# Performance work log

Hardware: AMD Instinct MI355X
Metric: run time of the kernel (lower is better)

Reference implementation:

```python
import jax, jax.numpy as jnp
import numpy as np

NUM_HEADS = 4
NUM_GROUPS = 32
EPS = 1e-5


def setup_inputs() -> dict:
    key = jax.random.key(0)
    ks = jax.random.split(key, 4)
    ch = 256
    x = jax.random.normal(ks[0], (16, ch, 32, 32), dtype=jnp.float32)
    gn_w = jnp.ones((ch,), jnp.float32)
    gn_b = jnp.zeros((ch,), jnp.float32)
    # conv1x1 weights, kaiming-ish scale
    qkv_w = jax.random.normal(ks[1], (3 * ch, ch), dtype=jnp.float32) / np.sqrt(ch)
    qkv_b = jnp.zeros((3 * ch,), jnp.float32)
    proj_w = jax.random.normal(ks[2], (ch, ch), dtype=jnp.float32) / np.sqrt(ch)
    proj_b = jnp.zeros((ch,), jnp.float32)
    return {"x": x, "gn_w": gn_w, "gn_b": gn_b, "qkv_w": qkv_w,
            "qkv_b": qkv_b, "proj_w": proj_w, "proj_b": proj_b}


def _group_norm(x, w, b):
    bsz, c, h, wd = x.shape
    g = NUM_GROUPS
    xg = x.reshape(bsz, g, c // g, h, wd)
    mean = xg.mean(axis=(2, 3, 4), keepdims=True)
    var = xg.var(axis=(2, 3, 4), keepdims=True)
    xg = (xg - mean) * jax.lax.rsqrt(var + EPS)
    return xg.reshape(bsz, c, h, wd) * w[None, :, None, None] + b[None, :, None, None]


def reference(x, gn_w, gn_b, qkv_w, qkv_b, proj_w, proj_b):
    b, c, h, w = x.shape
    hd = c // NUM_HEADS
    scale = hd ** (-0.5)
    y = _group_norm(x, gn_w, gn_b)
    # 1x1 conv == channel matmul
    qkv = jnp.einsum('oc,bchw->bohw', qkv_w, y) + qkv_b[None, :, None, None]
    q, k, v = jnp.split(qkv, 3, axis=1)
    q = q.reshape(b, NUM_HEADS, hd, h * w)
    k = k.reshape(b, NUM_HEADS, hd, h * w)
    v = v.reshape(b, NUM_HEADS, hd, h * w)
    attn = jnp.einsum('bhdi,bhdj->bhij', q * scale, k)
    attn = jax.nn.softmax(attn, axis=-1)
    out = jnp.einsum('bhij,bhdj->bhdi', attn, v)
    out = out.reshape(b, c, h, w)
    out = jnp.einsum('oc,bchw->bohw', proj_w, out) + proj_b[None, :, None, None]
    return x + out
```

## Files before the change

kernel.cpp:

```cpp
#include <hip/hip_runtime.h>
#include <cstddef>

#define B_   16
#define C_   256
#define HW_  1024
#define NH_  4
#define NG_  32
#define CPG_ 8
#define CS_  0.18033688f

typedef __attribute__((ext_vector_type(8))) short bf16x8;
typedef __attribute__((ext_vector_type(4))) short s16x4;
typedef __attribute__((ext_vector_type(8))) _Float16 f16x8;
typedef __attribute__((ext_vector_type(4))) float f32x4;

#define MFMA16B(a, b, c) __builtin_amdgcn_mfma_f32_16x16x32_bf16(a, b, c, 0, 0, 0)
#define MFMA16H(a, b, c) __builtin_amdgcn_mfma_f32_16x16x32_f16(a, b, c, 0, 0, 0)

#if __has_builtin(__builtin_amdgcn_mfma_f32_16x16x16bf16_1k)
#define HAVE_MFMA16K16 1
#define MFMA16B4(a, b, c) __builtin_amdgcn_mfma_f32_16x16x16bf16_1k(a, b, c, 0, 0, 0)
#else
#define HAVE_MFMA16K16 0
#endif

__device__ __forceinline__ float bf2f(unsigned short h) {
    unsigned int u = ((unsigned int)h) << 16;
    return __builtin_bit_cast(float, u);
}
__device__ __forceinline__ unsigned short f2bf(float f) {
    unsigned int u = __builtin_bit_cast(unsigned int, f);
    u += 0x7FFFu + ((u >> 16) & 1u);
    return (unsigned short)(u >> 16);
}
#if __has_builtin(__builtin_amdgcn_cvt_pk_bf16_f32)
__device__ __forceinline__ unsigned packbf(float a, float b) {
    auto v = __builtin_amdgcn_cvt_pk_bf16_f32(a, b);
    return __builtin_bit_cast(unsigned, v);
}
#else
__device__ __forceinline__ unsigned packbf(float a, float b) {
    unsigned ua = __builtin_bit_cast(unsigned, a) + 0x8000u;
    unsigned ub = __builtin_bit_cast(unsigned, b) + 0x8000u;
    return __builtin_amdgcn_perm(ub, ua, 0x07060302u);
}
#endif
__device__ __forceinline__ unsigned pkh(float a, float b) {
    auto h2 = __builtin_amdgcn_cvt_pkrtz(a, b);
    return __builtin_bit_cast(unsigned, h2);
}

__global__ __launch_bounds__(256) void gn_wcvt_kernel(
    const float* __restrict__ x,
    const float* __restrict__ gw,
    const float* __restrict__ gb,
    float2* __restrict__ scsh,
    const float* __restrict__ qw, const float* __restrict__ pw,
    unsigned short* __restrict__ oq, unsigned short* __restrict__ op)
{
    if (blockIdx.x >= 512) {
        int i = (blockIdx.x - 512) * 256 + threadIdx.x;
        const float* s; unsigned short* d; int j;
        if (i < 49152) { s = qw; d = oq; j = i; }
        else           { s = pw; d = op; j = i - 49152; }
        float4 f = ((const float4*)s)[j];
        uint2 u = {pkh(f.x, f.y), pkh(f.z, f.w)};
        *(uint2*)&d[(size_t)j * 4] = u;
        return;
    }
    int blk = blockIdx.x;
    const float* xg = x + (size_t)blk * CPG_ * HW_;
    const int N = CPG_ * HW_;

    float s = 0.f, ss = 0.f;
    for (int e = threadIdx.x * 4; e < N; e += 1024) {
        float4 v4 = *(const float4*)&xg[e];
        s  += v4.x + v4.y + v4.z + v4.w;
        ss += v4.x * v4.x + v4.y * v4.y + v4.z * v4.z + v4.w * v4.w;
    }
    #pragma unroll
    for (int off = 32; off > 0; off >>= 1) {
        s  += __shfl_down(s, off, 64);
        ss += __shfl_down(ss, off, 64);
    }
    __shared__ float red[8];
    __shared__ float2 stf;
    int lane = threadIdx.x & 63, wv = threadIdx.x >> 6;
    if (lane == 0) { red[wv] = s; red[4 + wv] = ss; }
    __syncthreads();
    if (threadIdx.x == 0) {
        float S  = red[0] + red[1] + red[2] + red[3];
        float SS = red[4] + red[5] + red[6] + red[7];
        float mean = S / (float)N;
        float var  = SS / (float)N - mean * mean;
        stf = make_float2(mean, rsqrtf(var + 1e-5f));
    }
    __syncthreads();
    if (threadIdx.x < 8) {
        int ch = (blk & 31) * CPG_ + threadIdx.x;
        float sc = stf.y * gw[ch];
        float sh = gb[ch] - stf.x * sc;
        scsh[blk * 8 + threadIdx.x] = make_float2(sc, sh);
    }
}

__global__ __launch_bounds__(256) void qkv_mfma_kernel(
    const unsigned short* __restrict__ W16,
    const float* __restrict__ Xf,
    const float* __restrict__ bias,
    const float2* __restrict__ scsh,
    unsigned short* __restrict__ qT,
    unsigned short* __restrict__ kT,
    unsigned short* __restrict__ vN)
{
    const int M = 768, K = 256, N = 1024;
    __shared__ union {
        struct { unsigned short A[2][128][40]; unsigned short Bt[2][64][40]; } st;
        unsigned short nd[2][64][72];
        unsigned short mn[128][72];
    } L;

    const int b  = blockIdx.z;
    const int m0 = blockIdx.y * 128, n0 = blockIdx.x * 64;
    const int t  = threadIdx.x;
    const int l15 = t & 15, quad = (t >> 4) & 3;
    const int wave = t >> 6, wm = wave >> 1, wn = wave & 1;

    union HF { uint4 q; f16x8 v; };

    f32x4 acc[4][2];
    #pragma unroll
    for (int mt = 0; mt < 4; ++mt)
        #pragma unroll
        for (int nt = 0; nt < 2; ++nt)
            acc[mt][nt] = (f32x4){0.f, 0.f, 0.f, 0.f};

    const int ar = t >> 1, akh = (t & 1) * 16;
    const int bn = t & 63, bkb = t >> 6;

    uint4 pa0, pa1;
    float pv[8];
    float2 ss[8];

    auto PREF = [&](int k0) {
        const unsigned short* wp = &W16[(size_t)(m0 + ar) * K + k0 + akh];
        pa0 = *(const uint4*)wp;
        pa1 = *(const uint4*)(wp + 8);
        int ch = k0 + bkb * 8;
        const float* xp = &Xf[((size_t)b * K + ch) * N + n0 + bn];
        #pragma unroll
        for (int j = 0; j < 8; ++j) pv[j] = xp[(size_t)j * N];
        const float4* sp = (const float4*)&scsh[b * C_ + ch];
        #pragma unroll
        for (int q2 = 0; q2 < 4; ++q2) ((float4*)ss)[q2] = sp[q2];
    };

    PREF(0);
    #pragma unroll 1
    for (int it = 0; it < 8; ++it) {
        const int bsel = it & 1;
        *(uint4*)&L.st.A[bsel][ar][akh]     = pa0;
        *(uint4*)&L.st.A[bsel][ar][akh + 8] = pa1;
        {
            float v[8];
            #pragma unroll
            for (int j = 0; j < 8; ++j) v[j] = pv[j] * ss[j].x + ss[j].y;
            uint4 bw = {pkh(v[0], v[1]), pkh(v[2], v[3]), pkh(v[4], v[5]), pkh(v[6], v[7])};
            *(uint4*)&L.st.Bt[bsel][bn][bkb * 8] = bw;
        }
        __syncthreads();
        if (it + 1 < 8) PREF((it + 1) * 32);
        HF af[4], bfv[2];
        #pragma unroll
        for (int mt = 0; mt < 4; ++mt)
            af[mt].q = *(const uint4*)&L.st.A[bsel][wm * 64 + mt * 16 + l15][quad * 8];
        #pragma unroll
        for (int nt = 0; nt < 2; ++nt)
            bfv[nt].q = *(const uint4*)&L.st.Bt[bsel][wn * 32 + nt * 16 + l15][quad * 8];
        #pragma unroll
        for (int mt = 0; mt < 4; ++mt)
            #pragma unroll
            for (int nt = 0; nt < 2; ++nt)
                acc[mt][nt] = MFMA16H(af[mt].v, bfv[nt].v, acc[mt][nt]);
    }
    __syncthreads();

    if (m0 < 512) {
        const float qsc = (m0 < 256) ? CS_ : 1.f;
        #pragma unroll
        for (int mt = 0; mt < 4; ++mt)
            #pragma unroll
            for (int rr = 0; rr < 4; ++rr) {
                int dl = mt * 16 + quad * 4 + rr;
                float bv = bias[m0 + wm * 64 + dl];
                #pragma unroll
                for (int nt = 0; nt < 2; ++nt)
                    L.nd[wm][wn * 32 + nt * 16 + l15][dl] = f2bf((acc[mt][nt][rr] + bv) * qsc);
            }
        __syncthreads();
        unsigned short* dst = (m0 < 256) ? qT : kT;
        int headbase = (m0 & 255) >> 6;
        int hl = t >> 7, tt = t & 127;
        int nl = tt >> 1, db = (tt & 1) * 32;
        const unsigned short* src = &L.nd[hl][nl][db];
        unsigned short* gp = &dst[(((size_t)(b * 4 + headbase + hl)) * 1024 + n0 + nl) * 64 + db];
        uint4 u0 = *(const uint4*)(src);
        uint4 u1 = *(const uint4*)(src + 8);
        uint4 u2 = *(const uint4*)(src + 16);
        uint4 u3 = *(const uint4*)(src + 24);
        *(uint4*)(gp)      = u0;
        *(uint4*)(gp + 8)  = u1;
        *(uint4*)(gp + 16) = u2;
        *(uint4*)(gp + 24) = u3;
    } else {
        #pragma unroll
        for (int mt = 0; mt < 4; ++mt)
            #pragma unroll
            for (int rr = 0; rr < 4; ++rr) {
                int ml = wm * 64 + mt * 16 + quad * 4 + rr;
                float bv = bias[m0 + ml];
                #pragma unroll
                for (int nt = 0; nt < 2; ++nt)
                    L.mn[ml][wn * 32 + nt * 16 + l15] = f2bf(acc[mt][nt][rr] + bv);
            }
        __syncthreads();
        int ml = t & 127, nb = t >> 7;
        const unsigned short* src = &L.mn[ml][nb * 32];
        unsigned short* gp = &vN[((size_t)b * 256 + (m0 - 512) + ml) * 1024 + n0 + nb * 32];
        uint4 u0 = *(const uint4*)(src);
        uint4 u1 = *(const uint4*)(src + 8);
        uint4 u2 = *(const uint4*)(src + 16);
        uint4 u3 = *(const uint4*)(src + 24);
        *(uint4*)(gp)      = u0;
        *(uint4*)(gp + 8)  = u1;
        *(uint4*)(gp + 16) = u2;
        *(uint4*)(gp + 24) = u3;
    }
}

__global__ __launch_bounds__(256) void proj_mfma_kernel(
    const unsigned short* __restrict__ W16,
    const unsigned short* __restrict__ OP,
    const float* __restrict__ LPp,
    const float* __restrict__ bias,
    const float* __restrict__ res,
    float* __restrict__ outF)
{
    const int M = 256, K = 256, N = 1024;
    __shared__ struct { unsigned short A[2][64][40]; unsigned short Bt[2][64][40]; } L;

    const int b  = blockIdx.z;
    const int m0 = blockIdx.y * 64, n0 = blockIdx.x * 64;
    const int t  = threadIdx.x;
    const int l15 = t & 15, quad = (t >> 4) & 3;
    const int wave = t >> 6, wm = wave >> 1, wn = wave & 1;

    union HF { uint4 q; f16x8 v; };

    f32x4 acc[2][2];
    #pragma unroll
    for (int mt = 0; mt < 2; ++mt)
        #pragma unroll
        for (int nt = 0; nt < 2; ++nt)
            acc[mt][nt] = (f32x4){0.f, 0.f, 0.f, 0.f};

    const int ar = t >> 2, akh = (t & 3) * 8;
    const int bn = t & 63, bkb = t >> 6;

    float rinv[4];
    {
        int n = n0 + bn;
        #pragma unroll
        for (int h = 0; h < 4; ++h) {
            float l0 = LPp[(size_t)(b * 4 + h) * 1024 + n];
            float l1 = LPp[(size_t)(64 + b * 4 + h) * 1024 + n];
            rinv[h] = 1.f / (l0 + l1);
        }
    }

    uint4 pa;
    unsigned short ph0[8], ph1[8];
    int pH = 0;

    auto PREF = [&](int k0) {
        pa = *(const uint4*)&W16[(size_t)(m0 + ar) * K + k0 + akh];
        int ch = k0 + bkb * 8;
        pH = ch >> 6;
        size_t base = ((size_t)(b * 4 + pH) * 64 + (ch & 63)) * 1024 + n0 + bn;
        #pragma unroll
        for (int j = 0; j < 8; ++j) {
            ph0[j] = OP[base + (size_t)j * 1024];
            ph1[j] = OP[(size_t)64 * 64 * 1024 + base + (size_t)j * 1024];
        }
    };

    PREF(0);
    #pragma unroll 1
    for (int it = 0; it < 8; ++it) {
        const int bsel = it & 1;
        *(uint4*)&L.A[bsel][ar][akh] = pa;
        {
            float ri = rinv[pH];
            float v[8];
            #pragma unroll
            for (int j = 0; j < 8; ++j)
                v[j] = (bf2f(ph0[j]) + bf2f(ph1[j])) * ri;
            uint4 bw = {pkh(v[0], v[1]), pkh(v[2], v[3]), pkh(v[4], v[5]), pkh(v[6], v[7])};
            *(uint4*)&L.Bt[bsel][bn][bkb * 8] = bw;
        }
        __syncthreads();
        if (it + 1 < 8) PREF((it + 1) * 32);
        HF af[2], bfv[2];
        #pragma unroll
        for (int mt = 0; mt < 2; ++mt)
            af[mt].q = *(const uint4*)&L.A[bsel][wm * 32 + mt * 16 + l15][quad * 8];
        #pragma unroll
        for (int nt = 0; nt < 2; ++nt)
            bfv[nt].q = *(const uint4*)&L.Bt[bsel][wn * 32 + nt * 16 + l15][quad * 8];
        #pragma unroll
        for (int mt = 0; mt < 2; ++mt)
            #pragma unroll
            for (int nt = 0; nt < 2; ++nt)
                acc[mt][nt] = MFMA16H(af[mt].v, bfv[nt].v, acc[mt][nt]);
    }

    #pragma unroll
    for (int mt = 0; mt < 2; ++mt) {
        #pragma unroll
        for (int rr = 0; rr < 4; ++rr) {
            int m = m0 + wm * 32 + mt * 16 + quad * 4 + rr;
            float bv = bias[m];
            #pragma unroll
            for (int nt = 0; nt < 2; ++nt) {
                int n = n0 + wn * 32 + nt * 16 + l15;
                size_t off = ((size_t)b * M + m) * (size_t)N + n;
                outF[off] = acc[mt][nt][rr] + bv + res[off];
            }
        }
    }
}

__global__ __launch_bounds__(256) void attn_mfma_kernel(
    const unsigned short* __restrict__ qT,
    const unsigned short* __restrict__ kT,
    const unsigned short* __restrict__ vN,
    unsigned short* __restrict__ OP,
    float* __restrict__ LP)
{
    __shared__ unsigned short Kt[2][64][72];
    __shared__ unsigned short Vs[2][64][72];

    const int t    = threadIdx.x;
    const int wv   = t >> 6;
    const int l15  = t & 15;
    const int quad = (t >> 4) & 3;
    const int bh   = blockIdx.x;
    const int i0   = blockIdx.y * 128;
    const int jh   = blockIdx.z;

    union FragU { uint4 q; unsigned u[4]; bf16x8 v; };

    FragU qf[2][2];
    {
        const unsigned short* qg = qT + (size_t)bh * (1024 * 64);
        int qrow = i0 + wv * 32 + l15;
        #pragma unroll
        for (int nt = 0; nt < 2; ++nt)
            #pragma unroll
            for (int kt = 0; kt < 2; ++kt)
                qf[nt][kt].q = *(const uint4*)&qg[(size_t)(qrow + nt * 16) * 64 + kt * 32 + quad * 8];
    }

    f32x4 accO[4][2];
    #pragma unroll
    for (int m = 0; m < 4; ++m)
        #pragma unroll
        for (int n = 0; n < 2; ++n)
            accO[m][n] = (f32x4){0.f, 0.f, 0.f, 0.f};
    float l_i[2] = {0.f, 0.f};
#if HAVE_MFMA16K16
    f32x4 accL[2] = {(f32x4){0.f, 0.f, 0.f, 0.f}, (f32x4){0.f, 0.f, 0.f, 0.f}};
    const s16x4 ones4 = {(short)0x3F80, (short)0x3F80, (short)0x3F80, (short)0x3F80};
#endif

    const unsigned short* kg = kT + (size_t)bh * (1024 * 64);
    const unsigned short* vg = vN + (size_t)bh * (64 * 1024);

    const int slbase = l15 + ((quad & 1) << 5);
    const bool upper = (t & 32) != 0;
    (void)slbase; (void)upper;
    const int sr = t >> 2, sc = (t & 3) * 16;

    uint4 kr0, kr1, vr0, vr1;
    {
        const int j0 = jh * 512;
        const unsigned short* kp = &kg[(size_t)(j0 + sr) * 64 + sc];
        const unsigned short* vp = &vg[(size_t)sr * 1024 + j0 + sc];
        kr0 = *(const uint4*)kp;  kr1 = *(const uint4*)(kp + 8);
        vr0 = *(const uint4*)vp;  vr1 = *(const uint4*)(vp + 8);
    }

    for (int it = 0; it < 8; ++it) {
        const int bsel = it & 1;
        *(uint4*)&Kt[bsel][sr][sc]     = kr0;
        *(uint4*)&Kt[bsel][sr][sc + 8] = kr1;
        *(uint4*)&Vs[bsel][sr][sc]     = vr0;
        *(uint4*)&Vs[bsel][sr][sc + 8] = vr1;
        __syncthreads();
        if (it < 7) {
            const int j0n = jh * 512 + (it + 1) * 64;
            const unsigned short* kp = &kg[(size_t)(j0n + sr) * 64 + sc];
            const unsigned short* vp = &vg[(size_t)sr * 1024 + j0n + sc];
            kr0 = *(const uint4*)kp;  kr1 = *(const uint4*)(kp + 8);
            vr0 = *(const uint4*)vp;  vr1 = *(const uint4*)(vp + 8);
        }

        f32x4 accS[4][2];
        #pragma unroll
        for (int mt = 0; mt < 4; ++mt) {
            FragU ak[2];
            #pragma unroll
            for (int kt = 0; kt < 2; ++kt)
                ak[kt].q = *(const uint4*)&Kt[bsel][mt * 16 + l15][kt * 32 + quad * 8];
            #pragma unroll
            for (int nt = 0; nt < 2; ++nt) {
                f32x4 z = (f32x4){0.f, 0.f, 0.f, 0.f};
                z = MFMA16B(ak[0].v, qf[nt][0].v, z);
                z = MFMA16B(ak[1].v, qf[nt][1].v, z);
                accS[mt][nt] = z;
            }
        }

#if HAVE_MFMA16K16
        union PB { unsigned u[2]; s16x4 v; };
        PB pb[4][2];
        #pragma unroll
        for (int mt = 0; mt < 4; ++mt)
            #pragma unroll
            for (int nt = 0; nt < 2; ++nt) {
                float p0 = exp2f(accS[mt][nt][0]);
                float p1 = exp2f(accS[mt][nt][1]);
                float p2 = exp2f(accS[mt][nt][2]);
                float p3 = exp2f(accS[mt][nt][3]);
                pb[mt][nt].u[0] = packbf(p0, p1);
                pb[mt][nt].u[1] = packbf(p2, p3);
            }
        #pragma unroll
        for (int mt = 0; mt < 4; ++mt)
            #pragma unroll
            for (int nt = 0; nt < 2; ++nt)
                accL[nt] = MFMA16B4(ones4, pb[mt][nt].v, accL[nt]);
        #pragma unroll
        for (int mtd = 0; mtd < 4; ++mtd) {
            union AV { uint2 d; s16x4 v; } av[4];
            #pragma unroll
            for (int mt = 0; mt < 4; ++mt)
                av[mt].d = *(const uint2*)&Vs[bsel][mtd * 16 + l15][mt * 16 + quad * 4];
            #pragma unroll
            for (int nt = 0; nt < 2; ++nt)
                #pragma unroll
                for (int mt = 0; mt < 4; ++mt)
                    accO[mtd][nt] = MFMA16B4(av[mt].v, pb[mt][nt].v, accO[mtd][nt]);
        }
#else
        float rs[2] = {0.f, 0.f};
        unsigned pk[4][2][2];
        #pragma unroll
        for (int mt = 0; mt < 4; ++mt)
            #pragma unroll
            for (int nt = 0; nt < 2; ++nt) {
                float p0 = exp2f(accS[mt][nt][0]);
                float p1 = exp2f(accS[mt][nt][1]);
                float p2 = exp2f(accS[mt][nt][2]);
                float p3 = exp2f(accS[mt][nt][3]);
                rs[nt] += (p0 + p1) + (p2 + p3);
                pk[mt][nt][0] = packbf(p0, p1);
                pk[mt][nt][1] = packbf(p2, p3);
            }
        #pragma unroll
        for (int nt = 0; nt < 2; ++nt) {
            float r = rs[nt];
            r += __shfl_xor(r, 16, 64);
            r += __shfl_xor(r, 32, 64);
            l_i[nt] += r;
        }
        FragU bfr[2][2];
        #pragma unroll
        for (int kt = 0; kt < 2; ++kt)
            #pragma unroll
            for (int nt = 0; nt < 2; ++nt)
                #pragma unroll
                for (int w4 = 0; w4 < 4; ++w4) {
                    int sl = slbase + ((w4 >> 1) << 4);
                    int lo = __shfl((int)pk[2 * kt + 0][nt][w4 & 1], sl, 64);
                    int hi = __shfl((int)pk[2 * kt + 1][nt][w4 & 1], sl, 64);
                    bfr[kt][nt].u[w4] = (unsigned)(upper ? hi : lo);
                }
        #pragma unroll
        for (int mtd = 0; mtd < 4; ++mtd) {
            FragU av[2];
            #pragma unroll
            for (int kt = 0; kt < 2; ++kt)
                av[kt].q = *(const uint4*)&Vs[bsel][mtd * 16 + l15][kt * 32 + quad * 8];
            #pragma unroll
            for (int nt = 0; nt < 2; ++nt) {
                accO[mtd][nt] = MFMA16B(av[0].v, bfr[0][nt].v, accO[mtd][nt]);
                accO[mtd][nt] = MFMA16B(av[1].v, bfr[1][nt].v, accO[mtd][nt]);
            }
        }
#endif
    }

#if HAVE_MFMA16K16
    l_i[0] = accL[0][0];
    l_i[1] = accL[1][0];
#endif

    unsigned short* ob = OP + ((size_t)jh * 64 + bh) * (64 * 1024) + i0 + wv * 32;
    #pragma unroll
    for (int mtd = 0; mtd < 4; ++mtd)
        #pragma unroll
        for (int nt = 0; nt < 2; ++nt)
            #pragma unroll
            for (int rr = 0; rr < 4; ++rr) {
                int d = mtd * 16 + quad * 4 + rr;
                ob[(size_t)d * 1024 + nt * 16 + l15] = f2bf(accO[mtd][nt][rr]);
            }
    if (quad == 0) {
        float* lp = &LP[((size_t)jh * 64 + bh) * 1024 + i0 + wv * 32 + l15];
        lp[0]  = l_i[0];
        lp[16] = l_i[1];
    }
}

extern "C" void kernel_launch(void* const* d_in, const int* in_sizes, int n_in,
                              void* d_out, int out_size, void* d_ws, size_t ws_size,
                              hipStream_t stream)
{
    const float* x      = (const float*)d_in[0];
    const float* gn_w   = (const float*)d_in[1];
    const float* gn_b   = (const float*)d_in[2];
    const float* qkv_w  = (const float*)d_in[3];
    const float* qkv_b  = (const float*)d_in[4];
    const float* proj_w = (const float*)d_in[5];
    const float* proj_b = (const float*)d_in[6];
    float* out = (float*)d_out;

    char* ws = (char*)d_ws;
    float2* scsh = (float2*)ws;
    unsigned short* w16q = (unsigned short*)(ws + 32768);
    unsigned short* w16p = w16q + 768 * 256;
    unsigned short* qT   = w16p + 256 * 256;
    unsigned short* kT   = qT + (size_t)B_ * NH_ * HW_ * 64;
    unsigned short* vN   = kT + (size_t)B_ * NH_ * HW_ * 64;
    unsigned short* OP   = vN + (size_t)B_ * C_ * HW_;
    float*          LP   = (float*)(OP + (size_t)2 * B_ * C_ * HW_);
    (void)in_sizes; (void)n_in; (void)out_size; (void)ws_size;

    gn_wcvt_kernel<<<dim3(768), 256, 0, stream>>>(
        x, gn_w, gn_b, scsh, qkv_w, proj_w, w16q, w16p);

    qkv_mfma_kernel<<<dim3(HW_ / 64, 6, B_), 256, 0, stream>>>(
        w16q, x, qkv_b, scsh, qT, kT, vN);

    attn_mfma_kernel<<<dim3(NH_ * B_, HW_ / 128, 2), 256, 0, stream>>>(qT, kT, vN, OP, LP);

    proj_mfma_kernel<<<dim3(HW_ / 64, C_ / 64, B_), 256, 0, stream>>>(
        w16p, OP, LP, proj_b, x, out);
}
```

Before: 149.5 us.

## Materialize normalized fp16 activations in GN kernel and widen QKV M-tile to 256

The group-norm kernel now applies scale/shift itself and writes an fp16 copy of the normalized input, so the QKV GEMM reads half-width activations instead of fp32 plus per-channel scale/shift. The QKV GEMM tile grows from 128 to 256 output rows, so each block covers a full Q, K or V section and reuses the loaded activation tile across more rows. The grid drops from 6 to 3 blocks per column. The cost is an extra read and write pass over the activations in the GN kernel, more LDS and accumulator registers per block, and half as many QKV blocks, which lowers occupancy.

```diff
diff --git a/kernel.cpp b/kernel.cpp
--- a/kernel.cpp
+++ b/kernel.cpp
@@ -54,7 +54,7 @@
     const float* __restrict__ x,
     const float* __restrict__ gw,
     const float* __restrict__ gb,
-    float2* __restrict__ scsh,
+    unsigned short* __restrict__ y16,
     const float* __restrict__ qw, const float* __restrict__ pw,
     unsigned short* __restrict__ oq, unsigned short* __restrict__ op)
 {
@@ -69,7 +69,8 @@
         return;
     }
     int blk = blockIdx.x;
-    const float* xg = x + (size_t)blk * CPG_ * HW_;
+    const size_t base = (size_t)blk * CPG_ * HW_;
+    const float* xg = x + base;
     const int N = CPG_ * HW_;
 
     float s = 0.f, ss = 0.f;
@@ -96,122 +97,120 @@
         stf = make_float2(mean, rsqrtf(var + 1e-5f));
     }
     __syncthreads();
-    if (threadIdx.x < 8) {
-        int ch = (blk & 31) * CPG_ + threadIdx.x;
-        float sc = stf.y * gw[ch];
-        float sh = gb[ch] - stf.x * sc;
-        scsh[blk * 8 + threadIdx.x] = make_float2(sc, sh);
+    float mean = stf.x, rstd = stf.y;
+    for (int e = threadIdx.x * 4; e < N; e += 1024) {
+        int ch = (blk & 31) * CPG_ + (e >> 10);
+        float sc = rstd * gw[ch];
+        float sh = gb[ch] - mean * sc;
+        float4 v4 = *(const float4*)&xg[e];
+        uint2 u;
+        u.x = pkh(v4.x * sc + sh, v4.y * sc + sh);
+        u.y = pkh(v4.z * sc + sh, v4.w * sc + sh);
+        *(uint2*)&y16[base + e] = u;
     }
 }
 
 __global__ __launch_bounds__(256) void qkv_mfma_kernel(
     const unsigned short* __restrict__ W16,
-    const float* __restrict__ Xf,
+    const unsigned short* __restrict__ y16,
     const float* __restrict__ bias,
-    const float2* __restrict__ scsh,
     unsigned short* __restrict__ qT,
     unsigned short* __restrict__ kT,
     unsigned short* __restrict__ vN)
 {
-    const int M = 768, K = 256, N = 1024;
+    const int K = 256, N = 1024;
     __shared__ union {
-        struct { unsigned short A[2][128][40]; unsigned short Bt[2][64][40]; } st;
-        unsigned short nd[2][64][72];
-        unsigned short mn[128][72];
+        struct { unsigned short A[2][256][40]; unsigned short Bt[2][64][40]; } st;
+        unsigned short nd[64][288];
+        unsigned short mn[256][72];
     } L;
 
     const int b  = blockIdx.z;
-    const int m0 = blockIdx.y * 128, n0 = blockIdx.x * 64;
+    const int m0 = blockIdx.y * 256, n0 = blockIdx.x * 64;
     const int t  = threadIdx.x;
     const int l15 = t & 15, quad = (t >> 4) & 3;
-    const int wave = t >> 6, wm = wave >> 1, wn = wave & 1;
+    const int wm = t >> 6;
 
     union HF { uint4 q; f16x8 v; };
 
-    f32x4 acc[4][2];
+    f32x4 acc[4][4];
     #pragma unroll
     for (int mt = 0; mt < 4; ++mt)
         #pragma unroll
-        for (int nt = 0; nt < 2; ++nt)
+        for (int nt = 0; nt < 4; ++nt)
             acc[mt][nt] = (f32x4){0.f, 0.f, 0.f, 0.f};
 
-    const int ar = t >> 1, akh = (t & 1) * 16;
     const int bn = t & 63, bkb = t >> 6;
 
-    uint4 pa0, pa1;
-    float pv[8];
-    float2 ss[8];
+    uint4 pa[4];
+    unsigned short ph[8];
 
     auto PREF = [&](int k0) {
-        const unsigned short* wp = &W16[(size_t)(m0 + ar) * K + k0 + akh];
-        pa0 = *(const uint4*)wp;
-        pa1 = *(const uint4*)(wp + 8);
+        const unsigned short* wp = &W16[(size_t)(m0 + t) * K + k0];
+        pa[0] = *(const uint4*)(wp);
+        pa[1] = *(const uint4*)(wp + 8);
+        pa[2] = *(const uint4*)(wp + 16);
+        pa[3] = *(const uint4*)(wp + 24);
         int ch = k0 + bkb * 8;
-        const float* xp = &Xf[((size_t)b * K + ch) * N + n0 + bn];
-        #pragma unroll
-        for (int j = 0; j < 8; ++j) pv[j] = xp[(size_t)j * N];
-        const float4* sp = (const float4*)&scsh[b * C_ + ch];
-        #pragma unroll
-        for (int q2 = 0; q2 < 4; ++q2) ((float4*)ss)[q2] = sp[q2];
+        const unsigned short* xp = &y16[((size_t)b * 256 + ch) * 1024 + n0 + bn];
+        #pragma unroll
+        for (int j = 0; j < 8; ++j) ph[j] = xp[(size_t)j * 1024];
     };
 
     PREF(0);
     #pragma unroll 1
     for (int it = 0; it < 8; ++it) {
         const int bsel = it & 1;
-        *(uint4*)&L.st.A[bsel][ar][akh]     = pa0;
-        *(uint4*)&L.st.A[bsel][ar][akh + 8] = pa1;
+        *(uint4*)&L.st.A[bsel][t][0]  = pa[0];
+        *(uint4*)&L.st.A[bsel][t][8]  = pa[1];
+        *(uint4*)&L.st.A[bsel][t][16] = pa[2];
+        *(uint4*)&L.st.A[bsel][t][24] = pa[3];
         {
-            float v[8];
-            #pragma unroll
-            for (int j = 0; j < 8; ++j) v[j] = pv[j] * ss[j].x + ss[j].y;
-            uint4 bw = {pkh(v[0], v[1]), pkh(v[2], v[3]), pkh(v[4], v[5]), pkh(v[6], v[7])};
+            uint4 bw;
+            bw.x = (unsigned)ph[0] | ((unsigned)ph[1] << 16);
+            bw.y = (unsigned)ph[2] | ((unsigned)ph[3] << 16);
+            bw.z = (unsigned)ph[4] | ((unsigned)ph[5] << 16);
+            bw.w = (unsigned)ph[6] | ((unsigned)ph[7] << 16);
             *(uint4*)&L.st.Bt[bsel][bn][bkb * 8] = bw;
         }
         __syncthreads();
         if (it + 1 < 8) PREF((it + 1) * 32);
-        HF af[4], bfv[2];
+        HF af[4], bfv[4];
         #pragma unroll
         for (int mt = 0; mt < 4; ++mt)
             af[mt].q = *(const uint4*)&L.st.A[bsel][wm * 64 + mt * 16 + l15][quad * 8];
         #pragma unroll
-        for (int nt = 0; nt < 2; ++nt)
-            bfv[nt].q = *(const uint4*)&L.st.Bt[bsel][wn * 32 + nt * 16 + l15][quad * 8];
-        #pragma unroll
-        for (int mt = 0; mt < 4; ++mt)
-            #pragma unroll
-            for (int nt = 0; nt < 2; ++nt)
+        for (int nt = 0; nt < 4; ++nt)
+            bfv[nt].q = *(const uint4*)&L.st.Bt[bsel][nt * 16 + l15][quad * 8];
+        #pragma unroll
+        for (int mt = 0; mt < 4; ++mt)
+            #pragma unroll
+            for (int nt = 0; nt < 4; ++nt)
                 acc[mt][nt] = MFMA16H(af[mt].v, bfv[nt].v, acc[mt][nt]);
     }
     __syncthreads();
 
     if (m0 < 512) {
-        const float qsc = (m0 < 256) ? CS_ : 1.f;
+        const float qsc = (m0 == 0) ? CS_ : 1.f;
         #pragma unroll
         for (int mt = 0; mt < 4; ++mt)
             #pragma unroll
             for (int rr = 0; rr < 4; ++rr) {
-                int dl = mt * 16 + quad * 4 + rr;
-                float bv = bias[m0 + wm * 64 + dl];
+                int ml = wm * 64 + mt * 16 + quad * 4 + rr;
+                float bv = bias[m0 + ml];
+                int skew = (ml >> 6) * 72 + (ml & 63);
                 #pragma unroll
-                for (int nt = 0; nt < 2; ++nt)
-                    L.nd[wm][wn * 32 + nt * 16 + l15][dl] = f2bf((acc[mt][nt][rr] + bv) * qsc);
+                for (int nt = 0; nt < 4; ++nt)
+                    L.nd[nt * 16 + l15][skew] = f2bf((acc[mt][nt][rr] + bv) * qsc);
             }
         __syncthreads();
-        unsigned short* dst = (m0 < 256) ? qT : kT;
-        int headbase = (m0 & 255) >> 6;
-        int hl = t >> 7, tt = t & 127;
-        int nl = tt >> 1, db = (tt & 1) * 32;
-        const unsigned short* src = &L.nd[hl][nl][db];
-        unsigned short* gp = &dst[(((size_t)(b * 4 + headbase + hl)) * 1024 + n0 + nl) * 64 + db];
-        uint4 u0 = *(const uint4*)(src);
-        uint4 u1 = *(const uint4*)(src + 8);
-        uint4 u2 = *(const uint4*)(src + 16);
-        uint4 u3 = *(const uint4*)(src + 24);
-        *(uint4*)(gp)      = u0;
-        *(uint4*)(gp + 8)  = u1;
-        *(uint4*)(gp + 16) = u2;
-        *(uint4*)(gp + 24) = u3;
+        unsigned short* dst = (m0 == 0) ? qT : kT;
+        int n = t >> 2, h = t & 3;
+        const unsigned short* src = &L.nd[n][h * 72];
+        unsigned short* gp = &dst[((size_t)(b * 4 + h) * 1024 + n0 + n) * 64];
+        #pragma unroll
+        for (int u = 0; u < 8; ++u)
+            *(uint4*)(gp + u * 8) = *(const uint4*)(src + u * 8);
     } else {
         #pragma unroll
         for (int mt = 0; mt < 4; ++mt)
@@ -220,21 +219,15 @@
                 int ml = wm * 64 + mt * 16 + quad * 4 + rr;
                 float bv = bias[m0 + ml];
                 #pragma unroll
-                for (int nt = 0; nt < 2; ++nt)
-                    L.mn[ml][wn * 32 + nt * 16 + l15] = f2bf(acc[mt][nt][rr] + bv);
+                for (int nt = 0; nt < 4; ++nt)
+                    L.mn[ml][nt * 16 + l15] = f2bf(acc[mt][nt][rr] + bv);
             }
         __syncthreads();
-        int ml = t & 127, nb = t >> 7;
-        const unsigned short* src = &L.mn[ml][nb * 32];
-        unsigned short* gp = &vN[((size_t)b * 256 + (m0 - 512) + ml) * 1024 + n0 + nb * 32];
-        uint4 u0 = *(const uint4*)(src);
-        uint4 u1 = *(const uint4*)(src + 8);
-        uint4 u2 = *(const uint4*)(src + 16);
-        uint4 u3 = *(const uint4*)(src + 24);
-        *(uint4*)(gp)      = u0;
-        *(uint4*)(gp + 8)  = u1;
-        *(uint4*)(gp + 16) = u2;
-        *(uint4*)(gp + 24) = u3;
+        const unsigned short* src = &L.mn[t][0];
+        unsigned short* gp = &vN[((size_t)b * 256 + t) * 1024 + n0];
+        #pragma unroll
+        for (int u = 0; u < 8; ++u)
+            *(uint4*)(gp + u * 8) = *(const uint4*)(src + u * 8);
     }
 }
 
@@ -547,8 +540,8 @@
     float* out = (float*)d_out;
 
     char* ws = (char*)d_ws;
-    float2* scsh = (float2*)ws;
-    unsigned short* w16q = (unsigned short*)(ws + 32768);
+    unsigned short* y16  = (unsigned short*)ws;
+    unsigned short* w16q = y16 + (size_t)B_ * C_ * HW_;
     unsigned short* w16p = w16q + 768 * 256;
     unsigned short* qT   = w16p + 256 * 256;
     unsigned short* kT   = qT + (size_t)B_ * NH_ * HW_ * 64;
@@ -558,10 +551,10 @@
     (void)in_sizes; (void)n_in; (void)out_size; (void)ws_size;
 
     gn_wcvt_kernel<<<dim3(768), 256, 0, stream>>>(
-        x, gn_w, gn_b, scsh, qkv_w, proj_w, w16q, w16p);
-
-    qkv_mfma_kernel<<<dim3(HW_ / 64, 6, B_), 256, 0, stream>>>(
-        w16q, x, qkv_b, scsh, qT, kT, vN);
+        x, gn_w, gn_b, y16, qkv_w, proj_w, w16q, w16p);
+
+    qkv_mfma_kernel<<<dim3(HW_ / 64, 3, B_), 256, 0, stream>>>(
+        w16q, y16, qkv_b, qT, kT, vN);
 
     attn_mfma_kernel<<<dim3(NH_ * B_, HW_ / 128, 2), 256, 0, stream>>>(qT, kT, vN, OP, LP);
 
```

Result: slower. 179.2 us (+19.9%).

## Materialize normalized fp16 activations in GroupNorm kernel for QKV GEMM

Applied to the files above, without the earlier changes.

The GroupNorm kernel now applies scale and shift itself and writes the normalized activations as fp16 to a workspace buffer, instead of only emitting per-channel scale/shift. The QKV GEMM then loads 2-byte fp16 values rather than fp32 x plus scale/shift, which halves its B-operand traffic across the six M-blocks that each reread x. In exchange, GroupNorm reads x a second time and writes an extra 8MB intermediate. The QKV loads stay strided 16-bit scalar loads.

```diff
diff --git a/kernel.cpp b/kernel.cpp
--- a/kernel.cpp
+++ b/kernel.cpp
@@ -54,7 +54,7 @@
     const float* __restrict__ x,
     const float* __restrict__ gw,
     const float* __restrict__ gb,
-    float2* __restrict__ scsh,
+    unsigned short* __restrict__ y16,
     const float* __restrict__ qw, const float* __restrict__ pw,
     unsigned short* __restrict__ oq, unsigned short* __restrict__ op)
 {
@@ -69,7 +69,8 @@
         return;
     }
     int blk = blockIdx.x;
-    const float* xg = x + (size_t)blk * CPG_ * HW_;
+    const size_t base = (size_t)blk * CPG_ * HW_;
+    const float* xg = x + base;
     const int N = CPG_ * HW_;
 
     float s = 0.f, ss = 0.f;
@@ -96,24 +97,28 @@
         stf = make_float2(mean, rsqrtf(var + 1e-5f));
     }
     __syncthreads();
-    if (threadIdx.x < 8) {
-        int ch = (blk & 31) * CPG_ + threadIdx.x;
-        float sc = stf.y * gw[ch];
-        float sh = gb[ch] - stf.x * sc;
-        scsh[blk * 8 + threadIdx.x] = make_float2(sc, sh);
+    float mean = stf.x, rstd = stf.y;
+    for (int e = threadIdx.x * 4; e < N; e += 1024) {
+        int ch = (blk & 31) * CPG_ + (e >> 10);
+        float sc = rstd * gw[ch];
+        float sh = gb[ch] - mean * sc;
+        float4 v4 = *(const float4*)&xg[e];
+        uint2 u;
+        u.x = pkh(v4.x * sc + sh, v4.y * sc + sh);
+        u.y = pkh(v4.z * sc + sh, v4.w * sc + sh);
+        *(uint2*)&y16[base + e] = u;
     }
 }
 
 __global__ __launch_bounds__(256) void qkv_mfma_kernel(
     const unsigned short* __restrict__ W16,
-    const float* __restrict__ Xf,
+    const unsigned short* __restrict__ y16,
     const float* __restrict__ bias,
-    const float2* __restrict__ scsh,
     unsigned short* __restrict__ qT,
     unsigned short* __restrict__ kT,
     unsigned short* __restrict__ vN)
 {
-    const int M = 768, K = 256, N = 1024;
+    const int K = 256, N = 1024;
     __shared__ union {
         struct { unsigned short A[2][128][40]; unsigned short Bt[2][64][40]; } st;
         unsigned short nd[2][64][72];
@@ -139,20 +144,16 @@
     const int bn = t & 63, bkb = t >> 6;
 
     uint4 pa0, pa1;
-    float pv[8];
-    float2 ss[8];
+    unsigned short ph[8];
 
     auto PREF = [&](int k0) {
         const unsigned short* wp = &W16[(size_t)(m0 + ar) * K + k0 + akh];
         pa0 = *(const uint4*)wp;
         pa1 = *(const uint4*)(wp + 8);
         int ch = k0 + bkb * 8;
-        const float* xp = &Xf[((size_t)b * K + ch) * N + n0 + bn];
-        #pragma unroll
-        for (int j = 0; j < 8; ++j) pv[j] = xp[(size_t)j * N];
-        const float4* sp = (const float4*)&scsh[b * C_ + ch];
-        #pragma unroll
-        for (int q2 = 0; q2 < 4; ++q2) ((float4*)ss)[q2] = sp[q2];
+        const unsigned short* xp = &y16[((size_t)b * 256 + ch) * 1024 + n0 + bn];
+        #pragma unroll
+        for (int j = 0; j < 8; ++j) ph[j] = xp[(size_t)j * 1024];
     };
 
     PREF(0);
@@ -162,10 +163,11 @@
         *(uint4*)&L.st.A[bsel][ar][akh]     = pa0;
         *(uint4*)&L.st.A[bsel][ar][akh + 8] = pa1;
         {
-            float v[8];
-            #pragma unroll
-            for (int j = 0; j < 8; ++j) v[j] = pv[j] * ss[j].x + ss[j].y;
-            uint4 bw = {pkh(v[0], v[1]), pkh(v[2], v[3]), pkh(v[4], v[5]), pkh(v[6], v[7])};
+            uint4 bw;
+            bw.x = (unsigned)ph[0] | ((unsigned)ph[1] << 16);
+            bw.y = (unsigned)ph[2] | ((unsigned)ph[3] << 16);
+            bw.z = (unsigned)ph[4] | ((unsigned)ph[5] << 16);
+            bw.w = (unsigned)ph[6] | ((unsigned)ph[7] << 16);
             *(uint4*)&L.st.Bt[bsel][bn][bkb * 8] = bw;
         }
         __syncthreads();
@@ -547,8 +549,8 @@
     float* out = (float*)d_out;
 
     char* ws = (char*)d_ws;
-    float2* scsh = (float2*)ws;
-    unsigned short* w16q = (unsigned short*)(ws + 32768);
+    unsigned short* y16  = (unsigned short*)ws;
+    unsigned short* w16q = y16 + (size_t)B_ * C_ * HW_;
     unsigned short* w16p = w16q + 768 * 256;
     unsigned short* qT   = w16p + 256 * 256;
     unsigned short* kT   = qT + (size_t)B_ * NH_ * HW_ * 64;
@@ -558,10 +560,10 @@
     (void)in_sizes; (void)n_in; (void)out_size; (void)ws_size;
 
     gn_wcvt_kernel<<<dim3(768), 256, 0, stream>>>(
-        x, gn_w, gn_b, scsh, qkv_w, proj_w, w16q, w16p);
+        x, gn_w, gn_b, y16, qkv_w, proj_w, w16q, w16p);
 
     qkv_mfma_kernel<<<dim3(HW_ / 64, 6, B_), 256, 0, stream>>>(
-        w16q, x, qkv_b, scsh, qT, kT, vN);
+        w16q, y16, qkv_b, qT, kT, vN);
 
     attn_mfma_kernel<<<dim3(NH_ * B_, HW_ / 128, 2), 256, 0, stream>>>(qT, kT, vN, OP, LP);
 
```

Result: no change. 147.6 us (-1.3%).
